# Optimization experiments

Hardware: AMD Instinct MI355X
Metric: run time of the kernel (lower is better)

Reference implementation:

```python
import jax, jax.numpy as jnp
import numpy as np

PW = 2        # positive_window
NM = 5        # negative_margin
TEMP = 0.1    # temperature
WEIGHT = 1.0
NEG_INF = -1e30


def setup_inputs() -> dict:
    key = jax.random.key(0)
    B, T, D = 64, 512, 1024
    hidden_states = jax.random.normal(key, (B, T, D), dtype=jnp.float32)
    return {"hidden_states": hidden_states}


def reference(hidden_states):
    B, T, D = hidden_states.shape
    # F.normalize(dim=-1): x / max(||x||, eps)
    norm = jnp.linalg.norm(hidden_states, axis=-1, keepdims=True)
    feats = hidden_states / jnp.maximum(norm, 1e-12)  # [B,T,D]

    # Only t with neg_start = t+NM < T-1 contribute a loss term.
    Tv = T - NM - 1                      # number of valid anchors
    t_idx = jnp.arange(Tv)               # [Tv]

    # positives: mean of feats at offsets {-PW..-1, 1..PW}, clipped to >=0
    offsets = jnp.concatenate([jnp.arange(-PW, 0), jnp.arange(1, PW + 1)])  # [2*PW]
    pos_idx = t_idx[:, None] + offsets[None, :]        # [Tv, 2*PW]
    pos_mask = (pos_idx >= 0) & (pos_idx < T)
    pos_idx_c = jnp.clip(pos_idx, 0, T - 1)
    pos_feats = feats[:, pos_idx_c]                    # [B, Tv, 2*PW, D]
    pos_cnt = pos_mask.sum(axis=1).astype(feats.dtype)  # [Tv]
    positives = (pos_feats * pos_mask[None, :, :, None].astype(feats.dtype)).sum(axis=2) \
                / pos_cnt[None, :, None]               # [B, Tv, D]

    anchors = feats[:, :Tv]                            # [B, Tv, D]
    pos_score = jnp.einsum('btd,btd->bt', anchors, positives) / TEMP   # [B, Tv]

    # negatives: feats[:, t+NM:] -> full scores masked where s < t+NM
    neg_scores = jnp.einsum('btd,bsd->bts', anchors, feats) / TEMP     # [B, Tv, T]
    s_idx = jnp.arange(T)
    neg_mask = s_idx[None, :] >= (t_idx[:, None] + NM)  # [Tv, T]
    neg_scores = jnp.where(neg_mask[None], neg_scores, NEG_INF)

    all_scores = jnp.concatenate([pos_score[:, :, None], neg_scores], axis=-1)  # [B, Tv, 1+T]
    # cross-entropy with label 0, averaged over batch per t, then over t
    loss_bt = jax.nn.logsumexp(all_scores, axis=-1) - pos_score  # [B, Tv]
    return loss_bt.mean() * WEIGHT
```

## Files before the change

kernel.cpp:

```cpp
#include <hip/hip_runtime.h>
#include <hip/hip_bf16.h>
#include <math.h>

constexpr int   Bc       = 64;
constexpr int   Tc       = 512;
constexpr int   Dc       = 1024;
constexpr int   NMc      = 5;
constexpr int   TvC      = Tc - NMc - 1;
constexpr float TEMP_INV = 10.0f;

using f32x4 = __attribute__((ext_vector_type(4))) float;
using i32x4 = __attribute__((ext_vector_type(4))) int;
using i32x8 = __attribute__((ext_vector_type(8))) int;

__device__ inline float wave_reduce_sum(float v) {
#pragma unroll
    for (int off = 32; off; off >>= 1) v += __shfl_xor(v, off);
    return v;
}

__device__ inline unsigned char f2e4m3(float f) {
    unsigned u = __float_as_uint(f);
    unsigned s = (u >> 24) & 0x80u;
    float a = __uint_as_float(u & 0x7fffffffu);
    if (a >= 448.f) return (unsigned char)(s | 0x7Eu);
    int Ef = (int)((u >> 23) & 0xFFu) - 127;
    unsigned r;
    if (Ef < -6) {
        int n = (int)rintf(a * 512.0f);
        r = (unsigned)n;
    } else {
        unsigned m23 = u & 0x7fffffu;
        unsigned m = (m23 + 0x7ffffu + ((m23 >> 20) & 1u)) >> 20;
        int E = Ef + 7;
        if (m == 8u) { m = 0u; E += 1; }
        r = ((unsigned)E << 3) | m;
    }
    return (unsigned char)(s | r);
}

#define GLOAD16(gp, lp)                                                        \
    __builtin_amdgcn_global_load_lds(                                          \
        (const __attribute__((address_space(1))) void*)(gp),                   \
        (__attribute__((address_space(3))) void*)(lp), 16, 0, 0)

__global__ __launch_bounds__(256) void tcl_prep(const float* __restrict__ h,
                                                unsigned char* __restrict__ fq,
                                                float* __restrict__ out) {
    if (blockIdx.x == 0 && threadIdx.x == 0) *out = 0.f;
    const int row  = blockIdx.x * 4 + (threadIdx.x >> 6);
    const int lane = threadIdx.x & 63;
    const float4* h4 = reinterpret_cast<const float4*>(h) + (size_t)row * 256 + lane;
    float4 v[4];
    float ss = 0.f;
#pragma unroll
    for (int i = 0; i < 4; ++i) {
        v[i] = h4[i * 64];
        ss += v[i].x*v[i].x + v[i].y*v[i].y + v[i].z*v[i].z + v[i].w*v[i].w;
    }
    ss = wave_reduce_sum(ss);
    const float inv = 1.0f / fmaxf(sqrtf(ss), 1e-12f);
    unsigned* o4 = reinterpret_cast<unsigned*>(fq + (size_t)row * Dc);
#pragma unroll
    for (int i = 0; i < 4; ++i) {
        const unsigned pk = (unsigned)f2e4m3(v[i].x * inv)
                          | ((unsigned)f2e4m3(v[i].y * inv) << 8)
                          | ((unsigned)f2e4m3(v[i].z * inv) << 16)
                          | ((unsigned)f2e4m3(v[i].w * inv) << 24);
        o4[lane + i * 64] = pk;
    }
}

__device__ __constant__ unsigned char JOB_TI[20] =
    {0,1, 0,1,2,3, 0,1,2,3,4,5, 0,1,2,3,4,5,6,7};
__device__ __constant__ unsigned char JOB_SJ[20] =
    {0,0, 1,1,1,1, 2,2,2,2,2,2, 3,3,3,3,3,3,3,3};

__global__ __launch_bounds__(256) void tcl_scores(const unsigned char* __restrict__ fq,
                                                  float* __restrict__ S_part,
                                                  float* __restrict__ pos_d,
                                                  float* __restrict__ pos_x) {
    const int p  = blockIdx.x;
    const int b  = (p & 7) * 8 + ((p >> 3) / 20);
    const int j  = (p >> 3) % 20;
    const int ti = (int)JOB_TI[j];
    const int sj = (int)JOB_SJ[j];
    const int t0 = ti * 64;
    const int s0 = sj * 128;
    const bool is_diag = (ti == 2 * sj) || (ti == 2 * sj + 1);
    const bool is_x    = (ti == 2 * sj - 1);

    const unsigned char* f = fq + (size_t)b * Tc * Dc;
    const int lane = threadIdx.x & 63;
    const int wid  = threadIdx.x >> 6;
    const int wr   = wid >> 1, wc = wid & 1;

    __shared__ __align__(16) unsigned char Als[64 * 128];
    __shared__ __align__(16) unsigned char Bls[128 * 128];

    const int sub = lane >> 3;
    const int c8  = lane & 7;
    const int cswb = (c8 ^ sub) << 4;
    const unsigned char* gA[2]; const unsigned char* gB[4];
    int lAo[2]; int lBo[4];
#pragma unroll
    for (int i = 0; i < 2; ++i) {
        const int ri = wid * 2 + i;
        gA[i] = f + (size_t)(t0 + ri * 8 + sub) * Dc + cswb;
        lAo[i] = ri * 1024;
    }
#pragma unroll
    for (int i = 0; i < 4; ++i) {
        const int ri = wid * 4 + i;
        gB[i] = f + (size_t)(s0 + ri * 8 + sub) * Dc + cswb;
        lBo[i] = ri * 1024;
    }

    const int r16 = lane & 15, kg = lane >> 4;
    const int xk  = r16 & 7;
    const int o0  = ((2 * kg)     ^ xk) << 4;
    const int o1  = ((2 * kg + 1) ^ xk) << 4;
    int aoff[2][2], boff[4][2];
#pragma unroll
    for (int q = 0; q < 2; ++q) {
        const int rb = (wr * 32 + q * 16 + r16) * 128;
        aoff[q][0] = rb + o0; aoff[q][1] = rb + o1;
    }
#pragma unroll
    for (int q = 0; q < 4; ++q) {
        const int rb = (wc * 64 + q * 16 + r16) * 128;
        boff[q][0] = rb + o0; boff[q][1] = rb + o1;
    }

    f32x4 acc[2][4];
#pragma unroll
    for (int fa = 0; fa < 2; ++fa)
#pragma unroll
        for (int fbj = 0; fbj < 4; ++fbj) acc[fa][fbj] = f32x4{0.f, 0.f, 0.f, 0.f};

    for (int kt = 0; kt < 8; ++kt) {
#pragma unroll
        for (int i = 0; i < 2; ++i) { GLOAD16(gA[i], Als + lAo[i]); gA[i] += 128; }
#pragma unroll
        for (int i = 0; i < 4; ++i) { GLOAD16(gB[i], Bls + lBo[i]); gB[i] += 128; }
        __syncthreads();

        i32x8 av[2], bv[4];
#pragma unroll
        for (int q = 0; q < 2; ++q) {
            i32x4 lo = *(const i32x4*)(Als + aoff[q][0]);
            i32x4 hi = *(const i32x4*)(Als + aoff[q][1]);
            av[q] = __builtin_shufflevector(lo, hi, 0, 1, 2, 3, 4, 5, 6, 7);
        }
#pragma unroll
        for (int q = 0; q < 4; ++q) {
            i32x4 lo = *(const i32x4*)(Bls + boff[q][0]);
            i32x4 hi = *(const i32x4*)(Bls + boff[q][1]);
            bv[q] = __builtin_shufflevector(lo, hi, 0, 1, 2, 3, 4, 5, 6, 7);
        }
#pragma unroll
        for (int fa = 0; fa < 2; ++fa)
#pragma unroll
            for (int fbj = 0; fbj < 4; ++fbj)
                acc[fa][fbj] = __builtin_amdgcn_mfma_scale_f32_16x16x128_f8f6f4(
                    av[fa], bv[fbj], acc[fa][fbj],
                    0, 0,
                    0, 0x7F7F7F7F,
                    0, 0x7F7F7F7F);
        __syncthreads();
    }

    __shared__ float S_sh[2][64];
    __shared__ float P_sh[2][64];
#pragma unroll
    for (int fa = 0; fa < 2; ++fa) {
#pragma unroll
        for (int r = 0; r < 4; ++r) {
            const int trow = t0 + wr * 32 + fa * 16 + kg * 4 + r;
            float v = 0.f, pv = 0.f;
#pragma unroll
            for (int fbj = 0; fbj < 4; ++fbj) {
                const int col = s0 + wc * 64 + fbj * 16 + r16;
                const float sc = acc[fa][fbj][r] * TEMP_INV;
                v += (col >= trow + NMc) ? __expf(sc - 10.f) : 0.f;
                const int dd = col - trow;
                pv += (dd * dd == 1 || dd * dd == 4) ? sc : 0.f;
            }
#pragma unroll
            for (int off = 1; off < 16; off <<= 1) {
                v  += __shfl_xor(v, off);
                pv += __shfl_xor(pv, off);
            }
            if (r16 == 0) {
                const int rl = wr * 32 + fa * 16 + kg * 4 + r;
                S_sh[wc][rl] = v;
                P_sh[wc][rl] = pv;
            }
        }
    }

    if (is_x && wr == 1 && wc == 0) {
        float cv = 0.f;
        const int c = s0 + r16;
#pragma unroll
        for (int fa = 0; fa < 2; ++fa)
#pragma unroll
            for (int r = 0; r < 4; ++r) {
                const int trow = t0 + 32 + fa * 16 + kg * 4 + r;
                const int dd = c - trow;
                cv += (dd == 1 || dd == 2) ? acc[fa][0][r] * TEMP_INV : 0.f;
            }
        cv += __shfl_xor(cv, 16);
        cv += __shfl_xor(cv, 32);
        if (kg == 0 && r16 < 2) pos_x[(size_t)b * Tc + c] = cv;
    }

    __syncthreads();
    if (threadIdx.x < 64) {
        const int t = t0 + threadIdx.x;
        S_part[((size_t)b * 4 + sj) * Tc + t] = S_sh[0][threadIdx.x] + S_sh[1][threadIdx.x];
        const float pr = P_sh[0][threadIdx.x] + P_sh[1][threadIdx.x];
        if (is_diag)
            pos_d[(size_t)b * Tc + t] = pr;
        if (is_x && threadIdx.x >= 62)
            pos_x[(size_t)b * Tc + t] = pr;
    }
}

__global__ __launch_bounds__(256) void tcl_combine(const float* __restrict__ S_part,
                                                   const float* __restrict__ pos_d,
                                                   const float* __restrict__ pos_x,
                                                   float* __restrict__ out, float scale) {
    const int b = blockIdx.x;
    float lsum = 0.f;
    for (int t = threadIdx.x; t < TvC; t += 256) {
        const int ti = t >> 7, tl = t & 127;
        float S = 0.f;
        for (int sj = ti; sj < 4; ++sj) S += S_part[((size_t)b * 4 + sj) * Tc + t];
        float praw = pos_d[(size_t)b * Tc + t];
        if ((tl >= 126 && ti < 3) || (tl <= 1 && ti > 0))
            praw += pos_x[(size_t)b * Tc + t];
        const float cnt = (t == 0) ? 2.f : (t == 1) ? 3.f : 4.f;
        const float pos = praw / cnt;
        lsum += __logf(__expf(pos - 10.f) + S) + 10.f - pos;
    }
    lsum = wave_reduce_sum(lsum);
    __shared__ float wls[4];
    const int lane = threadIdx.x & 63, wid = threadIdx.x >> 6;
    if (lane == 0) wls[wid] = lsum;
    __syncthreads();
    if (threadIdx.x == 0)
        atomicAdd(out, (wls[0] + wls[1] + wls[2] + wls[3]) * scale);
}

extern "C" void kernel_launch(void* const* d_in, const int* in_sizes, int n_in,
                              void* d_out, int out_size, void* d_ws, size_t ws_size,
                              hipStream_t stream) {
    const float* h = (const float*)d_in[0];
    float* out = (float*)d_out;

    const size_t feats_bytes = (size_t)Bc * Tc * Dc;
    const size_t spart_bytes = (size_t)Bc * 4 * Tc * sizeof(float);
    const size_t posd_bytes  = (size_t)Bc * Tc * sizeof(float);
    const float  scale       = 1.0f / (float)(Bc * TvC);

    unsigned char* fq = (unsigned char*)d_ws;
    float* S_part = (float*)((char*)d_ws + feats_bytes);
    float* pos_d  = (float*)((char*)d_ws + feats_bytes + spart_bytes);
    float* pos_x  = (float*)((char*)d_ws + feats_bytes + spart_bytes + posd_bytes);

    tcl_prep<<<Bc * Tc / 4, 256, 0, stream>>>(h, fq, out);
    tcl_scores<<<Bc * 20, 256, 0, stream>>>(fq, S_part, pos_d, pos_x);
    tcl_combine<<<Bc, 256, 0, stream>>>(S_part, pos_d, pos_x, out, scale);
    (void)ws_size; (void)in_sizes; (void)n_in; (void)out_size;
}
```

Baseline: 59.18 us.

## Use 64x64 score tiles with double-buffered LDS loads and manual waitcnt pipelining

The score kernel now uses 64x64 tiles (36 upper-triangular jobs per batch) instead of 64x128, which skips more masked work and launches more blocks. The K loop double-buffers LDS, issuing the next stage's async global-to-LDS loads while computing the current one, and uses explicit vmcnt and barrier waits in place of __syncthreads. The combine kernel and workspace layout are updated for 8 column partials. The trade-off is less reuse per block, more partial sums to combine, and fragile hand-written wait counts.

```diff
diff --git a/kernel.cpp b/kernel.cpp
--- a/kernel.cpp
+++ b/kernel.cpp
@@ -44,6 +44,11 @@
         (const __attribute__((address_space(1))) void*)(gp),                   \
         (__attribute__((address_space(3))) void*)(lp), 16, 0, 0)
 
+#define VW4()  asm volatile("s_waitcnt vmcnt(4)" ::: "memory")
+#define VW0()  asm volatile("s_waitcnt vmcnt(0)" ::: "memory")
+#define SBAR() asm volatile("s_barrier" ::: "memory")
+#define LBAR() asm volatile("s_waitcnt lgkmcnt(0)\n\ts_barrier" ::: "memory")
+
 __global__ __launch_bounds__(256) void tcl_prep(const float* __restrict__ h,
                                                 unsigned char* __restrict__ fq,
                                                 float* __restrict__ out) {
@@ -71,107 +76,109 @@
     }
 }
 
-__device__ __constant__ unsigned char JOB_TI[20] =
-    {0,1, 0,1,2,3, 0,1,2,3,4,5, 0,1,2,3,4,5,6,7};
-__device__ __constant__ unsigned char JOB_SJ[20] =
-    {0,0, 1,1,1,1, 2,2,2,2,2,2, 3,3,3,3,3,3,3,3};
-
-__global__ __launch_bounds__(256) void tcl_scores(const unsigned char* __restrict__ fq,
-                                                  float* __restrict__ S_part,
-                                                  float* __restrict__ pos_d,
-                                                  float* __restrict__ pos_x) {
+__device__ __constant__ unsigned char JOB_TI[36] =
+    {0,0,0,0,0,0,0,0, 1,1,1,1,1,1,1, 2,2,2,2,2,2, 3,3,3,3,3, 4,4,4,4, 5,5,5, 6,6, 7};
+__device__ __constant__ unsigned char JOB_SJ[36] =
+    {0,1,2,3,4,5,6,7, 1,2,3,4,5,6,7, 2,3,4,5,6,7, 3,4,5,6,7, 4,5,6,7, 5,6,7, 6,7, 7};
+
+__global__ __launch_bounds__(256, 5) void tcl_scores(const unsigned char* __restrict__ fq,
+                                                     float* __restrict__ S_part,
+                                                     float* __restrict__ pos_d,
+                                                     float* __restrict__ pos_x) {
     const int p  = blockIdx.x;
-    const int b  = (p & 7) * 8 + ((p >> 3) / 20);
-    const int j  = (p >> 3) % 20;
+    const int b  = (p & 7) * 8 + ((p >> 3) / 36);
+    const int j  = (p >> 3) % 36;
     const int ti = (int)JOB_TI[j];
     const int sj = (int)JOB_SJ[j];
     const int t0 = ti * 64;
-    const int s0 = sj * 128;
-    const bool is_diag = (ti == 2 * sj) || (ti == 2 * sj + 1);
-    const bool is_x    = (ti == 2 * sj - 1);
+    const int s0 = sj * 64;
+    const bool is_diag = (sj == ti);
+    const bool is_x    = (sj == ti + 1);
 
     const unsigned char* f = fq + (size_t)b * Tc * Dc;
     const int lane = threadIdx.x & 63;
     const int wid  = threadIdx.x >> 6;
     const int wr   = wid >> 1, wc = wid & 1;
 
-    __shared__ __align__(16) unsigned char Als[64 * 128];
-    __shared__ __align__(16) unsigned char Bls[128 * 128];
+    __shared__ __align__(16) unsigned char Als[2 * 64 * 128];
+    __shared__ __align__(16) unsigned char Bls[2 * 64 * 128];
 
     const int sub = lane >> 3;
     const int c8  = lane & 7;
     const int cswb = (c8 ^ sub) << 4;
-    const unsigned char* gA[2]; const unsigned char* gB[4];
-    int lAo[2]; int lBo[4];
+    const unsigned char* gA[2]; const unsigned char* gB[2];
+    int lAo[2], lBo[2];
 #pragma unroll
     for (int i = 0; i < 2; ++i) {
         const int ri = wid * 2 + i;
         gA[i] = f + (size_t)(t0 + ri * 8 + sub) * Dc + cswb;
+        gB[i] = f + (size_t)(s0 + ri * 8 + sub) * Dc + cswb;
         lAo[i] = ri * 1024;
-    }
-#pragma unroll
-    for (int i = 0; i < 4; ++i) {
-        const int ri = wid * 4 + i;
-        gB[i] = f + (size_t)(s0 + ri * 8 + sub) * Dc + cswb;
         lBo[i] = ri * 1024;
     }
+
+#define STAGE(BUF)                                                             \
+    do {                                                                       \
+        _Pragma("unroll")                                                      \
+        for (int i = 0; i < 2; ++i) {                                          \
+            GLOAD16(gA[i], Als + (BUF) * 8192 + lAo[i]); gA[i] += 128;         \
+            GLOAD16(gB[i], Bls + (BUF) * 8192 + lBo[i]); gB[i] += 128;         \
+        }                                                                      \
+    } while (0)
 
     const int r16 = lane & 15, kg = lane >> 4;
     const int xk  = r16 & 7;
     const int o0  = ((2 * kg)     ^ xk) << 4;
     const int o1  = ((2 * kg + 1) ^ xk) << 4;
-    int aoff[2][2], boff[4][2];
+    int aoff[2][2], boff[2][2];
 #pragma unroll
     for (int q = 0; q < 2; ++q) {
-        const int rb = (wr * 32 + q * 16 + r16) * 128;
-        aoff[q][0] = rb + o0; aoff[q][1] = rb + o1;
-    }
-#pragma unroll
-    for (int q = 0; q < 4; ++q) {
-        const int rb = (wc * 64 + q * 16 + r16) * 128;
+        const int ra = (wr * 32 + q * 16 + r16) * 128;
+        const int rb = (wc * 32 + q * 16 + r16) * 128;
+        aoff[q][0] = ra + o0; aoff[q][1] = ra + o1;
         boff[q][0] = rb + o0; boff[q][1] = rb + o1;
     }
 
-    f32x4 acc[2][4];
+    f32x4 acc[2][2];
 #pragma unroll
     for (int fa = 0; fa < 2; ++fa)
 #pragma unroll
-        for (int fbj = 0; fbj < 4; ++fbj) acc[fa][fbj] = f32x4{0.f, 0.f, 0.f, 0.f};
-
-    for (int kt = 0; kt < 8; ++kt) {
-#pragma unroll
-        for (int i = 0; i < 2; ++i) { GLOAD16(gA[i], Als + lAo[i]); gA[i] += 128; }
-#pragma unroll
-        for (int i = 0; i < 4; ++i) { GLOAD16(gB[i], Bls + lBo[i]); gB[i] += 128; }
-        __syncthreads();
-
-        i32x8 av[2], bv[4];
-#pragma unroll
-        for (int q = 0; q < 2; ++q) {
-            i32x4 lo = *(const i32x4*)(Als + aoff[q][0]);
-            i32x4 hi = *(const i32x4*)(Als + aoff[q][1]);
-            av[q] = __builtin_shufflevector(lo, hi, 0, 1, 2, 3, 4, 5, 6, 7);
-        }
-#pragma unroll
-        for (int q = 0; q < 4; ++q) {
-            i32x4 lo = *(const i32x4*)(Bls + boff[q][0]);
-            i32x4 hi = *(const i32x4*)(Bls + boff[q][1]);
-            bv[q] = __builtin_shufflevector(lo, hi, 0, 1, 2, 3, 4, 5, 6, 7);
-        }
-#pragma unroll
-        for (int fa = 0; fa < 2; ++fa)
-#pragma unroll
-            for (int fbj = 0; fbj < 4; ++fbj)
-                acc[fa][fbj] = __builtin_amdgcn_mfma_scale_f32_16x16x128_f8f6f4(
-                    av[fa], bv[fbj], acc[fa][fbj],
-                    0, 0,
-                    0, 0x7F7F7F7F,
-                    0, 0x7F7F7F7F);
-        __syncthreads();
-    }
-
-    __shared__ float S_sh[2][64];
-    __shared__ float P_sh[2][64];
+        for (int fbj = 0; fbj < 2; ++fbj) acc[fa][fbj] = f32x4{0.f, 0.f, 0.f, 0.f};
+
+#define COMPUTE(BUF)                                                           \
+    do {                                                                       \
+        i32x8 av[2], bv[2];                                                    \
+        _Pragma("unroll")                                                      \
+        for (int q = 0; q < 2; ++q) {                                          \
+            i32x4 alo = *(const i32x4*)(Als + (BUF) * 8192 + aoff[q][0]);      \
+            i32x4 ahi = *(const i32x4*)(Als + (BUF) * 8192 + aoff[q][1]);      \
+            av[q] = __builtin_shufflevector(alo, ahi, 0,1,2,3,4,5,6,7);        \
+            i32x4 blo = *(const i32x4*)(Bls + (BUF) * 8192 + boff[q][0]);      \
+            i32x4 bhi = *(const i32x4*)(Bls + (BUF) * 8192 + boff[q][1]);      \
+            bv[q] = __builtin_shufflevector(blo, bhi, 0,1,2,3,4,5,6,7);        \
+        }                                                                      \
+        _Pragma("unroll")                                                      \
+        for (int fa = 0; fa < 2; ++fa)                                         \
+            _Pragma("unroll")                                                  \
+            for (int fbj = 0; fbj < 2; ++fbj)                                  \
+                acc[fa][fbj] = __builtin_amdgcn_mfma_scale_f32_16x16x128_f8f6f4(\
+                    av[fa], bv[fbj], acc[fa][fbj],                             \
+                    0, 0, 0, 0x7F7F7F7F, 0, 0x7F7F7F7F);                       \
+    } while (0)
+
+    STAGE(0);
+    STAGE(1);
+    for (int i = 0; i < 3; ++i) {
+        VW4(); SBAR(); COMPUTE(0); LBAR(); STAGE(0);
+        VW4(); SBAR(); COMPUTE(1); LBAR(); STAGE(1);
+    }
+    VW4(); SBAR(); COMPUTE(0); LBAR();
+    VW0(); SBAR(); COMPUTE(1);
+#undef STAGE
+#undef COMPUTE
+
+    float* S_sh = (float*)Als;
+    float* P_sh = (float*)(Als + 512);
 #pragma unroll
     for (int fa = 0; fa < 2; ++fa) {
 #pragma unroll
@@ -179,8 +186,8 @@
             const int trow = t0 + wr * 32 + fa * 16 + kg * 4 + r;
             float v = 0.f, pv = 0.f;
 #pragma unroll
-            for (int fbj = 0; fbj < 4; ++fbj) {
-                const int col = s0 + wc * 64 + fbj * 16 + r16;
+            for (int fbj = 0; fbj < 2; ++fbj) {
+                const int col = s0 + wc * 32 + fbj * 16 + r16;
                 const float sc = acc[fa][fbj][r] * TEMP_INV;
                 v += (col >= trow + NMc) ? __expf(sc - 10.f) : 0.f;
                 const int dd = col - trow;
@@ -193,8 +200,8 @@
             }
             if (r16 == 0) {
                 const int rl = wr * 32 + fa * 16 + kg * 4 + r;
-                S_sh[wc][rl] = v;
-                P_sh[wc][rl] = pv;
+                S_sh[wc * 64 + rl] = v;
+                P_sh[wc * 64 + rl] = pv;
             }
         }
     }
@@ -218,8 +225,8 @@
     __syncthreads();
     if (threadIdx.x < 64) {
         const int t = t0 + threadIdx.x;
-        S_part[((size_t)b * 4 + sj) * Tc + t] = S_sh[0][threadIdx.x] + S_sh[1][threadIdx.x];
-        const float pr = P_sh[0][threadIdx.x] + P_sh[1][threadIdx.x];
+        S_part[((size_t)b * 8 + sj) * Tc + t] = S_sh[threadIdx.x] + S_sh[64 + threadIdx.x];
+        const float pr = P_sh[threadIdx.x] + P_sh[64 + threadIdx.x];
         if (is_diag)
             pos_d[(size_t)b * Tc + t] = pr;
         if (is_x && threadIdx.x >= 62)
@@ -234,11 +241,11 @@
     const int b = blockIdx.x;
     float lsum = 0.f;
     for (int t = threadIdx.x; t < TvC; t += 256) {
-        const int ti = t >> 7, tl = t & 127;
+        const int ti = t >> 6, tl = t & 63;
         float S = 0.f;
-        for (int sj = ti; sj < 4; ++sj) S += S_part[((size_t)b * 4 + sj) * Tc + t];
+        for (int sj = ti; sj < 8; ++sj) S += S_part[((size_t)b * 8 + sj) * Tc + t];
         float praw = pos_d[(size_t)b * Tc + t];
-        if ((tl >= 126 && ti < 3) || (tl <= 1 && ti > 0))
+        if ((tl >= 62 && ti < 7) || (tl <= 1 && ti > 0))
             praw += pos_x[(size_t)b * Tc + t];
         const float cnt = (t == 0) ? 2.f : (t == 1) ? 3.f : 4.f;
         const float pos = praw / cnt;
@@ -260,7 +267,7 @@
     float* out = (float*)d_out;
 
     const size_t feats_bytes = (size_t)Bc * Tc * Dc;
-    const size_t spart_bytes = (size_t)Bc * 4 * Tc * sizeof(float);
+    const size_t spart_bytes = (size_t)Bc * 8 * Tc * sizeof(float);
     const size_t posd_bytes  = (size_t)Bc * Tc * sizeof(float);
     const float  scale       = 1.0f / (float)(Bc * TvC);
 
@@ -270,7 +277,7 @@
     float* pos_x  = (float*)((char*)d_ws + feats_bytes + spart_bytes + posd_bytes);
 
     tcl_prep<<<Bc * Tc / 4, 256, 0, stream>>>(h, fq, out);
-    tcl_scores<<<Bc * 20, 256, 0, stream>>>(fq, S_part, pos_d, pos_x);
+    tcl_scores<<<Bc * 36, 256, 0, stream>>>(fq, S_part, pos_d, pos_x);
     tcl_combine<<<Bc, 256, 0, stream>>>(S_part, pos_d, pos_x, out, scale);
     (void)ws_size; (void)in_sizes; (void)n_in; (void)out_size;
 }
```

Result: slower. 62.98 us (+6.4%).
